# Kernel optimization log

Measured on AMD Instinct MI355X. Metric: run time of the kernel, lower is better.

The kernel has to match this reference:

```python
import jax, jax.numpy as jnp
import numpy as np

B, K, D, H = 4, 2048, 1024, 16
NCTX = K // 2
IMAGE_SIZE = 224
MAX_POS = 1024


def _build_rope_cache_2d(max_pos, dim, base=10000.0):
    half_dim = dim // 2
    theta = 1.0 / base ** (np.arange(0, half_dim, 2, dtype=np.float32) / half_dim)
    positions = np.arange(max_pos, dtype=np.float32)
    freqs = np.outer(positions, theta)  # [max_pos, dim/4]
    return jnp.asarray(np.stack([np.cos(freqs), np.sin(freqs)], axis=-1))  # [max_pos, dim/4, 2]


def apply_rope_2d(x, coords, rope_cache, image_size):
    b, k, d = x.shape
    half, quarter = d // 2, d // 4
    max_pos = rope_cache.shape[0]
    cn = jnp.clip(coords / image_size * (max_pos - 1), 0, max_pos - 1)
    y_pos = cn[..., 0].astype(jnp.int32)
    x_pos = cn[..., 1].astype(jnp.int32)
    y_rope = rope_cache[y_pos]  # [b,k,quarter,2]
    x_rope = rope_cache[x_pos]

    def rot(part, r):
        c, s = r[..., 0], r[..., 1]
        p0, p1 = part[..., 0], part[..., 1]
        return jnp.stack([p0 * c - p1 * s, p0 * s + p1 * c], -1).reshape(b, k, half)

    xp = x[..., :half].reshape(b, k, quarter, 2)
    yp = x[..., half:].reshape(b, k, quarter, 2)
    return jnp.concatenate([rot(xp, x_rope), rot(yp, y_rope)], -1)


def mha(q_tok, kv_tok, in_w, in_b, out_w, out_b, num_heads):
    b, nq, d = q_tok.shape
    hd = d // num_heads
    wq, wk, wv = jnp.split(in_w, 3, axis=0)
    bq, bk, bv = jnp.split(in_b, 3)
    q = (q_tok @ wq.T + bq).reshape(b, nq, num_heads, hd)
    k = (kv_tok @ wk.T + bk).reshape(b, -1, num_heads, hd)
    v = (kv_tok @ wv.T + bv).reshape(b, -1, num_heads, hd)
    s = jnp.einsum('bqhd,bkhd->bhqk', q, k) / jnp.sqrt(jnp.asarray(hd, q.dtype))
    a = jax.nn.softmax(s, axis=-1)
    o = jnp.einsum('bhqk,bkhd->bqhd', a, v).reshape(b, nq, d)
    return o @ out_w.T + out_b


def setup_inputs() -> dict:
    key = jax.random.key(0)
    ks = jax.random.split(key, 12)
    sc = 1.0 / np.sqrt(D)
    x = jax.random.normal(ks[0], (B, K, D), jnp.float32)
    coords = jax.random.uniform(ks[1], (B, K, 2), jnp.float32) * IMAGE_SIZE
    # boolean context mask with exactly NCTX context tokens per batch (code assumes equal counts)
    perms = jax.vmap(lambda k_: jax.random.permutation(k_, K))(jax.random.split(ks[2], B))
    is_context = jax.vmap(lambda m, i: m.at[i].set(True))(jnp.zeros((B, K), bool), perms[:, :NCTX])
    rope_cache = _build_rope_cache_2d(MAX_POS, D)
    return {
        'x': x, 'coords': coords, 'is_context': is_context, 'rope_cache': rope_cache,
        'ctx_in_w': jax.random.normal(ks[3], (3 * D, D), jnp.float32) * sc,
        'ctx_in_b': jnp.zeros((3 * D,), jnp.float32),
        'ctx_out_w': jax.random.normal(ks[4], (D, D), jnp.float32) * sc,
        'ctx_out_b': jnp.zeros((D,), jnp.float32),
        'tgt_in_w': jax.random.normal(ks[5], (3 * D, D), jnp.float32) * sc,
        'tgt_in_b': jnp.zeros((3 * D,), jnp.float32),
        'tgt_out_w': jax.random.normal(ks[6], (D, D), jnp.float32) * sc,
        'tgt_out_b': jnp.zeros((D,), jnp.float32),
    }


def reference(x, coords, is_context, rope_cache,
              ctx_in_w, ctx_in_b, ctx_out_w, ctx_out_b,
              tgt_in_w, tgt_in_b, tgt_out_w, tgt_out_b):
    # 2D RoPE before attention (as in the backbone)
    xr = apply_rope_2d(x, coords, rope_cache, IMAGE_SIZE)
    # stable argsort: context positions (key 0) first, in original order
    order = jnp.argsort(jnp.where(is_context, 0, 1), axis=1, stable=True)
    ctx_idx = order[:, :NCTX]   # [B, NCTX]
    tgt_idx = order[:, NCTX:]   # [B, K-NCTX]
    ctx_tok = jnp.take_along_axis(xr, ctx_idx[..., None], axis=1)
    tgt_tok = jnp.take_along_axis(xr, tgt_idx[..., None], axis=1)
    ctx_out = mha(ctx_tok, ctx_tok, ctx_in_w, ctx_in_b, ctx_out_w, ctx_out_b, H)
    tgt_out = mha(tgt_tok, ctx_tok, tgt_in_w, tgt_in_b, tgt_out_w, tgt_out_b, H)
    out = jnp.zeros_like(x)
    out = jax.vmap(lambda o, i, v: o.at[i].set(v))(out, ctx_idx, ctx_out)
    out = jax.vmap(lambda o, i, v: o.at[i].set(v))(out, tgt_idx, tgt_out)
    return out
```

## Files before the change

### kernel.cpp

```cpp
#include <hip/hip_runtime.h>
#include <math.h>

#define B_    4
#define K_    2048
#define D_    1024
#define H_    16
#define NCTX_ 1024

typedef unsigned short ushort_t;
typedef _Float16 f16;
typedef __attribute__((ext_vector_type(8))) _Float16 f16x8;
typedef __attribute__((ext_vector_type(4))) float f32x4;

union U4 {
  f16 h[4];
  ushort4 u;
};

union P4 {
  f16 h[4];
  ushort4 u;
};

__device__ __forceinline__ void gload16(const void* g, void* l) {
  __builtin_amdgcn_global_load_lds(
      (const __attribute__((address_space(1))) unsigned int*)g,
      (__attribute__((address_space(3))) unsigned int*)l, 16, 0, 0);
}

__global__ __launch_bounds__(256) void partition_kernel(
    const unsigned char* __restrict__ isctx, int* __restrict__ pos,
    int* __restrict__ ipos) {
  const int b = blockIdx.x;
  const int tid = threadIdx.x;
  const int wid = tid >> 6, lane = tid & 63;
  __shared__ int csum[4];
  __shared__ int waveTot[4];
  __shared__ int strideSh;

  int cnt = 0;
  for (int i = 0; i < 32; ++i) cnt += (isctx[tid * 32 + i] != 0);
  for (int off = 32; off; off >>= 1) cnt += __shfl_down(cnt, off, 64);
  if (lane == 0) csum[wid] = cnt;
  __syncthreads();
  if (tid == 0) {
    int t = csum[0] + csum[1] + csum[2] + csum[3];
    strideSh = (t > 2048) ? 1 : ((t > 768) ? 4 : 8);
  }
  __syncthreads();
  const int stride = strideSh;

  const unsigned char* base = isctx + (size_t)b * K_ * stride;
  int f[8];
  int s = 0;
  for (int i = 0; i < 8; ++i) {
    f[i] = base[(size_t)(tid * 8 + i) * stride] != 0;
    s += f[i];
  }
  int inc = s;
  for (int off = 1; off < 64; off <<= 1) {
    int v = __shfl_up(inc, off, 64);
    if (lane >= off) inc += v;
  }
  if (lane == 63) waveTot[wid] = inc;
  __syncthreads();
  int wOff = 0;
  for (int w = 0; w < wid; ++w) wOff += waveTot[w];
  int run = wOff + inc - s;
  for (int i = 0; i < 8; ++i) {
    int k = tid * 8 + i;
    int p;
    if (f[i]) {
      p = run;
      run++;
    } else {
      p = NCTX_ + k - run;
    }
    pos[b * K_ + k] = p;
    ipos[b * K_ + p] = k;
  }
}

__global__ __launch_bounds__(256) void rope_kernel(
    const float* __restrict__ x, const float* __restrict__ coords,
    const float* __restrict__ cache, const int* __restrict__ ipos,
    f16* __restrict__ tok) {
  const int row = blockIdx.x;
  const int b = row >> 11;
  const int r = row & (K_ - 1);
  const int k = ipos[row];
  const int t = threadIdx.x;

  const float cy = coords[(size_t)(b * K_ + k) * 2 + 0];
  const float cx = coords[(size_t)(b * K_ + k) * 2 + 1];
  const int ypos = (int)fminf(fmaxf(cy / 224.0f * 1023.0f, 0.0f), 1023.0f);
  const int xpos = (int)fminf(fmaxf(cx / 224.0f * 1023.0f, 0.0f), 1023.0f);

  const float4 v = ((const float4*)(x + ((size_t)b * K_ + k) * D_))[t];
  const int e = 4 * t;
  const float* crow;
  int coff;
  if (e < 512) {
    crow = cache + (size_t)xpos * 512;
    coff = e;
  } else {
    crow = cache + (size_t)ypos * 512;
    coff = e - 512;
  }
  const float4 cs = *(const float4*)(crow + coff);
  float o[4];
  o[0] = v.x * cs.x - v.y * cs.y;
  o[1] = v.x * cs.y + v.y * cs.x;
  o[2] = v.z * cs.z - v.w * cs.w;
  o[3] = v.z * cs.w + v.w * cs.z;
  U4 h;
#pragma unroll
  for (int i = 0; i < 4; ++i) h.h[i] = (f16)o[i];
  ((ushort4*)(tok + ((size_t)b * K_ + r) * D_))[t] = h.u;
}

__global__ __launch_bounds__(256) void cvt_all(
    const float* __restrict__ ctx_in_w, const float* __restrict__ tgt_in_w,
    const float* __restrict__ ctx_out_w, const float* __restrict__ tgt_out_w,
    f16* __restrict__ dst) {
  const int i4 = blockIdx.x * 256 + threadIdx.x;
  const int f = i4 * 4;
  const float* src;
  if (f < 3145728) src = ctx_in_w + f;
  else if (f < 5242880) src = tgt_in_w + (f - 3145728 + 1048576);
  else if (f < 6291456) src = tgt_in_w + (f - 5242880);
  else if (f < 7340032) src = ctx_out_w + (f - 6291456);
  else src = tgt_out_w + (f - 7340032);
  const float4 v = *(const float4*)src;
  U4 u;
  u.h[0] = (f16)v.x;
  u.h[1] = (f16)v.y;
  u.h[2] = (f16)v.z;
  u.h[3] = (f16)v.w;
  ((ushort4*)dst)[i4] = u.u;
}

#define GEMM_PRE(AP, WP, Kd)                                                  \
  const int rb_ = wave * 8 + (lane >> 3);          \
  const int kk_ = ((lane & 7) ^ (lane >> 3)) * 8;   \
  const f16* gA_ = (AP) + (size_t)rb_ * (Kd) + kk_;                           \
  const f16* gW_ = (WP) + (size_t)rb_ * (Kd) + kk_;                           \
  const int lA_ = wave * 8 * 64 + lane * 8;

#define GEMM_STAGE(k0s, bb)                                                   \
  _Pragma("unroll") for (int j = 0; j < 4; ++j) {                             \
    gload16(gA_ + (size_t)j * 32 * Kd_ + (k0s), &lds[(bb) + j * 2048 + lA_]); \
    gload16(gW_ + (size_t)j * 32 * Kd_ + (k0s),                               \
            &lds[(bb) + 8192 + j * 2048 + lA_]);                              \
  }

#define GEMM_TILE(bb)                                                         \
  _Pragma("unroll") for (int kh = 0; kh < 2; ++kh) {                          \
    f16x8 af[4], wf[4];                                                       \
    _Pragma("unroll") for (int i = 0; i < 4; ++i) {                           \
      const int ca = ((kh * 4 + quad) ^ (m16 & 7)) * 8;                       \
      af[i] = *(const f16x8*)&lds[(bb) + (wm + i * 16 + m16) * 64 + ca];      \
      wf[i] =                                                                 \
          *(const f16x8*)&lds[(bb) + 8192 + (wn + i * 16 + m16) * 64 + ca];   \
    }                                                                         \
    _Pragma("unroll") for (int i = 0; i < 4; ++i)                             \
        _Pragma("unroll") for (int j = 0; j < 4; ++j)                         \
      acc[i][j] = __builtin_amdgcn_mfma_f32_16x16x32_f16(af[i], wf[j],        \
                                                         acc[i][j], 0, 0, 0); \
  }

#define GEMM_CORE(AP, WP, Kd)                                                 \
  f32x4 acc[4][4];                                                            \
  {                                                                           \
    const f32x4 z = {0.f, 0.f, 0.f, 0.f};                                     \
    for (int i = 0; i < 4; ++i)                                               \
      for (int j = 0; j < 4; ++j) acc[i][j] = z;                              \
  }                                                                           \
  const int Kd_ = (Kd);                                                       \
  GEMM_PRE(AP, WP, Kd_)                                                       \
  GEMM_STAGE(0, 0)                                                            \
  for (int t = 0; t < Kd_ / 64; ++t) {                                        \
    const int cb = (t & 1) * 16384;                                           \
    if (t + 1 < Kd_ / 64) {                                                   \
      GEMM_STAGE((t + 1) * 64, ((t + 1) & 1) * 16384)                         \
      asm volatile("s_waitcnt vmcnt(8)" ::: "memory");                        \
    } else {                                                                  \
      asm volatile("s_waitcnt vmcnt(0)" ::: "memory");                        \
    }                                                                         \
    __builtin_amdgcn_s_barrier();                                             \
    asm volatile("" ::: "memory");                                            \
    GEMM_TILE(cb)                                                             \
    asm volatile("" ::: "memory");                                            \
    __builtin_amdgcn_s_barrier();                                             \
  }

__global__ __launch_bounds__(256, 2) void gemm_proj(
    const f16* __restrict__ tok, const f16* __restrict__ wcat,
    const float* __restrict__ ctx_in_b, const float* __restrict__ tgt_in_b,
    f16* __restrict__ qkvc, f16* __restrict__ kvt, f16* __restrict__ qt,
    f16* __restrict__ vtc, f16* __restrict__ vtt) {
  __shared__ f16 lds[32768];
  const int tid = threadIdx.x;
  const int wave = tid >> 6, lane = tid & 63;
  const int quad = lane >> 4, m16 = lane & 15;
  const int nb = blockIdx.x, mb = blockIdx.y, b = blockIdx.z;
  const int wm = (wave & 1) << 6, wn = (wave >> 1) << 6;
  const int m0 = mb * 128;
  const bool isQ = nb >= 40;
  const int n0 = isQ ? (nb - 40) * 128 : nb * 128;
  const f16* AP = tok + (size_t)b * K_ * D_ +
                  (isQ ? (size_t)NCTX_ * D_ : (size_t)0) + (size_t)m0 * D_;
  const f16* WP = wcat + (isQ ? (size_t)5242880 : (size_t)0) +
                  (size_t)n0 * D_;

  GEMM_CORE(AP, WP, D_)

#pragma unroll
  for (int j = 0; j < 4; ++j) {
    const int col = n0 + wn + j * 16 + m16;
    if (isQ) {
      const float bv = tgt_in_b[col];
      f16* dst = qt + (size_t)b * NCTX_ * 1024;
#pragma unroll
      for (int i = 0; i < 4; ++i) {
        const int mr = m0 + wm + i * 16 + quad * 4;
#pragma unroll
        for (int r = 0; r < 4; ++r)
          dst[(size_t)(mr + r) * 1024 + col] = (f16)(acc[i][j][r] + bv);
      }
    } else if (col < 2048) {
      const float bv = ctx_in_b[col];
      f16* dst = qkvc + (size_t)b * NCTX_ * 2048;
#pragma unroll
      for (int i = 0; i < 4; ++i) {
        const int mr = m0 + wm + i * 16 + quad * 4;
#pragma unroll
        for (int r = 0; r < 4; ++r)
          dst[(size_t)(mr + r) * 2048 + col] = (f16)(acc[i][j][r] + bv);
      }
    } else if (col >= 3072 && col < 4096) {
      const float bv = tgt_in_b[D_ + col - 3072];
      f16* dst = kvt + (size_t)b * NCTX_ * 1024;
      const int dcol = col - 3072;
#pragma unroll
      for (int i = 0; i < 4; ++i) {
        const int mr = m0 + wm + i * 16 + quad * 4;
#pragma unroll
        for (int r = 0; r < 4; ++r)
          dst[(size_t)(mr + r) * 1024 + dcol] = (f16)(acc[i][j][r] + bv);
      }
    } else {
      const bool isCtxV = col < 3072;
      const int hd = isCtxV ? (col - 2048) : (col - 4096);
      const float bv = isCtxV ? ctx_in_b[col] : tgt_in_b[D_ + col - 3072];
      f16* dst = (isCtxV ? vtc : vtt) +
                 ((size_t)(b * H_ + (hd >> 6)) << 16) +
                 (size_t)(hd & 63) * 1024;
#pragma unroll
      for (int i = 0; i < 4; ++i) {
        const int mr = m0 + wm + i * 16 + quad * 4;
        P4 p4;
#pragma unroll
        for (int r = 0; r < 4; ++r) p4.h[r] = (f16)(acc[i][j][r] + bv);
        *(ushort4*)(dst + mr) = p4.u;
      }
    }
  }
}

__global__ __launch_bounds__(256, 2) void gemm_out(
    const f16* __restrict__ Atok, const f16* __restrict__ Wbase,
    const float* __restrict__ bias_ctx, const float* __restrict__ bias_tgt,
    const int* __restrict__ ipos, float* __restrict__ out) {
  __shared__ f16 lds[32768];
  const int tid = threadIdx.x;
  const int wave = tid >> 6, lane = tid & 63;
  const int quad = lane >> 4, m16 = lane & 15;
  const int n0 = blockIdx.x * 128, m0 = blockIdx.y * 128;
  const int b = blockIdx.z & 3, sel = blockIdx.z >> 2;
  const int wm = (wave & 1) << 6, wn = (wave >> 1) << 6;
  const f16* AP = Atok + (size_t)b * K_ * D_ + (size_t)sel * NCTX_ * D_ +
                  (size_t)m0 * D_;
  const f16* WP = Wbase + (size_t)sel * 1048576 + (size_t)n0 * D_;
  const float* bias = sel ? bias_tgt : bias_ctx;

  GEMM_CORE(AP, WP, D_)

#pragma unroll
  for (int j = 0; j < 4; ++j) {
    const int col = n0 + wn + j * 16 + m16;
    const float bv = bias[col];
#pragma unroll
    for (int i = 0; i < 4; ++i) {
      const int mr = m0 + wm + i * 16 + quad * 4;
#pragma unroll
      for (int r = 0; r < 4; ++r) {
        const int orow = ipos[b * K_ + sel * NCTX_ + mr + r];
        out[(size_t)b * K_ * D_ + (size_t)orow * D_ + col] =
            acc[i][j][r] + bv;
      }
    }
  }
}

__global__ __launch_bounds__(512) void attn_mfma(
    const f16* __restrict__ qkvc, const f16* __restrict__ kvt,
    const f16* __restrict__ qt, const f16* __restrict__ vtc,
    const f16* __restrict__ vtt, f16* __restrict__ O) {
  __shared__ f16 QP[8192];
  __shared__ f16 Xb[12288];
  const int tid = threadIdx.x, wave = tid >> 6, lane = tid & 63;
  const int quad = lane >> 4, m16 = lane & 15;

  const int id = blockIdx.x;
  const int xcd = id & 7;
  const int t_ = id >> 3;
  const int j_ = t_ & 7;
  const int g = ((t_ >> 3) << 3) + xcd;
  const int h = g & 15;
  const int zz = g >> 4;
  const int b = zz & 3;
  const bool isCtx = zz < 4;
  const int q0 = j_ * 128;

  const f16* Qb;
  const f16* Kb;
  int ld;
  if (isCtx) {
    Qb = qkvc + (size_t)b * NCTX_ * 2048 + h * 64;
    Kb = Qb + 1024;
    ld = 2048;
  } else {
    Qb = qt + (size_t)b * NCTX_ * 1024 + h * 64;
    Kb = kvt + (size_t)b * NCTX_ * 1024 + h * 64;
    ld = 1024;
  }
  const f16* Vb = (isCtx ? vtc : vtt) + ((size_t)(b * H_ + h) << 16);
  f16* Ob = O + (size_t)b * K_ * D_ + (isCtx ? 0 : (size_t)NCTX_ * D_);

  const int rowS = tid >> 3;
  const int kkc = ((tid & 7) ^ (rowS & 7)) * 8;
  const int lB = tid * 8;

#pragma unroll
  for (int j = 0; j < 2; ++j)
    gload16(Qb + (size_t)(q0 + j * 64 + rowS) * ld + kkc, &QP[j * 4096 + lB]);
  gload16(Kb + (size_t)rowS * ld + kkc, &Xb[lB]);
  gload16(Vb + (size_t)rowS * 1024 + kkc, &Xb[4096 + lB]);

  float m_run = -1e30f, l_run = 0.f;
  f32x4 Oa[4];
  const f32x4 z = {0.f, 0.f, 0.f, 0.f};
#pragma unroll
  for (int j = 0; j < 4; ++j) Oa[j] = z;

  asm volatile("s_waitcnt vmcnt(0)" ::: "memory");
  __builtin_amdgcn_s_barrier();

  const int c0 = (quad ^ (m16 & 7)) * 8;
  const int c1 = ((quad + 4) ^ (m16 & 7)) * 8;
  const f16x8 qf0 = *(const f16x8*)&QP[(wave * 16 + m16) * 64 + c0];
  const f16x8 qf1 = *(const f16x8*)&QP[(wave * 16 + m16) * 64 + c1];

  f16* Pw = QP + wave * 1024;

  int xK = 0, xV = 4096;
  for (int kt = 0; kt < 16; ++kt) {
    int xKn = xK + 8192;
    if (xKn >= 12288) xKn -= 12288;

    asm volatile("s_waitcnt vmcnt(0)" ::: "memory");
    __builtin_amdgcn_s_barrier();
    asm volatile("" ::: "memory");
    if (kt < 15)
      gload16(Kb + (size_t)((kt + 1) * 64 + rowS) * ld + kkc, &Xb[xKn + lB]);

    f32x4 S[4];
    __builtin_amdgcn_s_setprio(1);
#pragma unroll
    for (int jn = 0; jn < 4; ++jn) {
      S[jn] = z;
      const f16x8 kf0 = *(const f16x8*)&Xb[xK + (jn * 16 + m16) * 64 + c0];
      const f16x8 kf1 = *(const f16x8*)&Xb[xK + (jn * 16 + m16) * 64 + c1];
      S[jn] = __builtin_amdgcn_mfma_f32_16x16x32_f16(kf0, qf0, S[jn], 0, 0, 0);
      S[jn] = __builtin_amdgcn_mfma_f32_16x16x32_f16(kf1, qf1, S[jn], 0, 0, 0);
    }
    __builtin_amdgcn_s_setprio(0);

    __builtin_amdgcn_s_barrier();
    asm volatile("" ::: "memory");
    if (kt < 15)
      gload16(Vb + (size_t)rowS * 1024 + (kt + 1) * 64 + kkc, &Xb[xK + lB]);

    float mv0 = fmaxf(fmaxf(S[0][0], S[1][0]), fmaxf(S[2][0], S[3][0]));
    float mv1 = fmaxf(fmaxf(S[0][1], S[1][1]), fmaxf(S[2][1], S[3][1]));
    float mv2 = fmaxf(fmaxf(S[0][2], S[1][2]), fmaxf(S[2][2], S[3][2]));
    float mv3 = fmaxf(fmaxf(S[0][3], S[1][3]), fmaxf(S[2][3], S[3][3]));
    float mx = fmaxf(fmaxf(mv0, mv1), fmaxf(mv2, mv3));
    mx = fmaxf(mx, __shfl_xor(mx, 16, 64));
    mx = fmaxf(mx, __shfl_xor(mx, 32, 64));
    mx *= 0.125f;

    const bool grow = !__all(mx <= m_run);
    float al = 1.f;
    if (grow) {
      const float mnew = fmaxf(m_run, mx);
      al = __expf(m_run - mnew);
      m_run = mnew;
    }

    float rs = 0.f;
#pragma unroll
    for (int jn = 0; jn < 4; ++jn) {
      P4 p4;
#pragma unroll
      for (int r = 0; r < 4; ++r) {
        const float p = __expf(__builtin_fmaf(S[jn][r], 0.125f, -m_run));
        rs += p;
        p4.h[r] = (f16)p;
      }
      *(ushort4*)&Pw[m16 * 64 + (((jn * 2 + (quad >> 1)) ^ (m16 & 7)) * 8) +
                     (quad & 1) * 4] = p4.u;
    }
    rs += __shfl_xor(rs, 16, 64);
    rs += __shfl_xor(rs, 32, 64);

    if (grow) {
      l_run = l_run * al + rs;
      float alq[4];
#pragma unroll
      for (int r = 0; r < 4; ++r) alq[r] = __shfl(al, quad * 4 + r, 64);
#pragma unroll
      for (int j = 0; j < 4; ++j) {
        Oa[j][0] *= alq[0];
        Oa[j][1] *= alq[1];
        Oa[j][2] *= alq[2];
        Oa[j][3] *= alq[3];
      }
    } else {
      l_run += rs;
    }

    const f16x8 pf0 = *(const f16x8*)&Pw[m16 * 64 + c0];
    const f16x8 pf1 = *(const f16x8*)&Pw[m16 * 64 + c1];
    __builtin_amdgcn_s_setprio(1);
#pragma unroll
    for (int jd = 0; jd < 4; ++jd) {
      const f16x8 vf0 = *(const f16x8*)&Xb[xV + (jd * 16 + m16) * 64 + c0];
      const f16x8 vf1 = *(const f16x8*)&Xb[xV + (jd * 16 + m16) * 64 + c1];
      Oa[jd] = __builtin_amdgcn_mfma_f32_16x16x32_f16(pf0, vf0, Oa[jd], 0, 0, 0);
      Oa[jd] = __builtin_amdgcn_mfma_f32_16x16x32_f16(pf1, vf1, Oa[jd], 0, 0, 0);
    }
    __builtin_amdgcn_s_setprio(0);

    xV = xK;
    xK = xKn;
  }

  float lq[4];
#pragma unroll
  for (int r = 0; r < 4; ++r) lq[r] = 1.0f / __shfl(l_run, quad * 4 + r, 64);
#pragma unroll
  for (int jd = 0; jd < 4; ++jd)
#pragma unroll
    for (int r = 0; r < 4; ++r) {
      const float v = Oa[jd][r] * lq[r];
      const size_t off = (size_t)(q0 + wave * 16 + quad * 4 + r) * D_ +
                         h * 64 + jd * 16 + m16;
      Ob[off] = (f16)v;
    }
}

extern "C" void kernel_launch(void* const* d_in, const int* in_sizes, int n_in,
                              void* d_out, int out_size, void* d_ws,
                              size_t ws_size, hipStream_t stream) {
  const float* x = (const float*)d_in[0];
  const float* coords = (const float*)d_in[1];
  const unsigned char* isctx = (const unsigned char*)d_in[2];
  const float* rope = (const float*)d_in[3];
  const float* ctx_in_w = (const float*)d_in[4];
  const float* ctx_in_b = (const float*)d_in[5];
  const float* ctx_out_w = (const float*)d_in[6];
  const float* ctx_out_b = (const float*)d_in[7];
  const float* tgt_in_w = (const float*)d_in[8];
  const float* tgt_in_b = (const float*)d_in[9];
  const float* tgt_out_w = (const float*)d_in[10];
  const float* tgt_out_b = (const float*)d_in[11];
  float* out = (float*)d_out;

  f16* ws = (f16*)d_ws;
  f16* tok = ws;
  f16* wcat = tok + 8388608;
  f16* qkvc = wcat + 8388608;
  f16* kvt = qkvc + 8388608;
  f16* qt = kvt + 4194304;
  f16* vtc = qt + 4194304;
  f16* vtt = vtc + 4194304;
  int* pos = (int*)(vtt + 4194304);
  int* ipos = pos + B_ * K_;

  partition_kernel<<<B_, 256, 0, stream>>>(isctx, pos, ipos);
  cvt_all<<<8192, 256, 0, stream>>>(ctx_in_w, tgt_in_w, ctx_out_w, tgt_out_w,
                                    wcat);
  rope_kernel<<<B_ * K_, 256, 0, stream>>>(x, coords, rope, ipos, tok);

  gemm_proj<<<dim3(48, 8, B_), 256, 0, stream>>>(
      tok, wcat, ctx_in_b, tgt_in_b, qkvc, kvt, qt, vtc, vtt);

  attn_mfma<<<dim3(1024, 1, 1), 512, 0, stream>>>(qkvc, kvt, qt, vtc, vtt,
                                                  tok);

  gemm_out<<<dim3(8, 8, 2 * B_), 256, 0, stream>>>(
      tok, wcat + 6291456, ctx_out_b, tgt_out_b, ipos, out);
}
```

Measured before the change: 278.8 us.

## Double-buffer K/V with 128-key tiles in attention kernel

Replaces the rotating three-slot K/V buffer and 64-key steps with separate double buffers for K and V over 128-key tiles. Each iteration prefetches the whole next tile, so only one barrier is needed per iteration instead of two, and the loop runs half as many times. The softmax max and rescale are now computed once per 128 keys. In exchange, LDS use rises from about 40KB to 80KB per block, which may cut occupancy, and more S registers are live at once. The P·V product is still done in two 64-key halves through the same per-wave P scratch.

```diff
diff --git a/kernel.cpp b/kernel.cpp
--- a/kernel.cpp
+++ b/kernel.cpp
@@ -308,7 +308,8 @@
     const f16* __restrict__ qt, const f16* __restrict__ vtc,
     const f16* __restrict__ vtt, f16* __restrict__ O) {
   __shared__ f16 QP[8192];
-  __shared__ f16 Xb[12288];
+  __shared__ f16 KB[2][8192];
+  __shared__ f16 VB[2][8192];
   const int tid = threadIdx.x, wave = tid >> 6, lane = tid & 63;
   const int quad = lane >> 4, m16 = lane & 15;
 
@@ -345,8 +346,11 @@
 #pragma unroll
   for (int j = 0; j < 2; ++j)
     gload16(Qb + (size_t)(q0 + j * 64 + rowS) * ld + kkc, &QP[j * 4096 + lB]);
-  gload16(Kb + (size_t)rowS * ld + kkc, &Xb[lB]);
-  gload16(Vb + (size_t)rowS * 1024 + kkc, &Xb[4096 + lB]);
+#pragma unroll
+  for (int j = 0; j < 2; ++j) {
+    gload16(Kb + (size_t)(j * 64 + rowS) * ld + kkc, &KB[0][j * 4096 + lB]);
+    gload16(Vb + (size_t)rowS * 1024 + j * 64 + kkc, &VB[0][j * 4096 + lB]);
+  }
 
   float m_run = -1e30f, l_run = 0.f;
   f32x4 Oa[4];
@@ -354,7 +358,7 @@
 #pragma unroll
   for (int j = 0; j < 4; ++j) Oa[j] = z;
 
-  asm volatile("s_waitcnt vmcnt(0)" ::: "memory");
+  asm volatile("s_waitcnt vmcnt(4)" ::: "memory");
   __builtin_amdgcn_s_barrier();
 
   const int c0 = (quad ^ (m16 & 7)) * 8;
@@ -364,39 +368,46 @@
 
   f16* Pw = QP + wave * 1024;
 
-  int xK = 0, xV = 4096;
-  for (int kt = 0; kt < 16; ++kt) {
-    int xKn = xK + 8192;
-    if (xKn >= 12288) xKn -= 12288;
+  for (int kt = 0; kt < 8; ++kt) {
+    const int cur = kt & 1;
 
     asm volatile("s_waitcnt vmcnt(0)" ::: "memory");
     __builtin_amdgcn_s_barrier();
     asm volatile("" ::: "memory");
-    if (kt < 15)
-      gload16(Kb + (size_t)((kt + 1) * 64 + rowS) * ld + kkc, &Xb[xKn + lB]);
-
-    f32x4 S[4];
+    if (kt < 7) {
+#pragma unroll
+      for (int j = 0; j < 2; ++j) {
+        gload16(Kb + (size_t)((kt + 1) * 128 + j * 64 + rowS) * ld + kkc,
+                &KB[cur ^ 1][j * 4096 + lB]);
+        gload16(Vb + (size_t)rowS * 1024 + (kt + 1) * 128 + j * 64 + kkc,
+                &VB[cur ^ 1][j * 4096 + lB]);
+      }
+    }
+
+    f32x4 S[8];
     __builtin_amdgcn_s_setprio(1);
 #pragma unroll
-    for (int jn = 0; jn < 4; ++jn) {
+    for (int jn = 0; jn < 8; ++jn) {
       S[jn] = z;
-      const f16x8 kf0 = *(const f16x8*)&Xb[xK + (jn * 16 + m16) * 64 + c0];
-      const f16x8 kf1 = *(const f16x8*)&Xb[xK + (jn * 16 + m16) * 64 + c1];
+      const f16x8 kf0 = *(const f16x8*)&KB[cur][(jn >> 2) * 4096 +
+                                               ((jn & 3) * 16 + m16) * 64 +
+                                               c0];
+      const f16x8 kf1 = *(const f16x8*)&KB[cur][(jn >> 2) * 4096 +
+                                               ((jn & 3) * 16 + m16) * 64 +
+                                               c1];
       S[jn] = __builtin_amdgcn_mfma_f32_16x16x32_f16(kf0, qf0, S[jn], 0, 0, 0);
       S[jn] = __builtin_amdgcn_mfma_f32_16x16x32_f16(kf1, qf1, S[jn], 0, 0, 0);
     }
     __builtin_amdgcn_s_setprio(0);
 
-    __builtin_amdgcn_s_barrier();
-    asm volatile("" ::: "memory");
-    if (kt < 15)
-      gload16(Vb + (size_t)rowS * 1024 + (kt + 1) * 64 + kkc, &Xb[xK + lB]);
-
-    float mv0 = fmaxf(fmaxf(S[0][0], S[1][0]), fmaxf(S[2][0], S[3][0]));
-    float mv1 = fmaxf(fmaxf(S[0][1], S[1][1]), fmaxf(S[2][1], S[3][1]));
-    float mv2 = fmaxf(fmaxf(S[0][2], S[1][2]), fmaxf(S[2][2], S[3][2]));
-    float mv3 = fmaxf(fmaxf(S[0][3], S[1][3]), fmaxf(S[2][3], S[3][3]));
-    float mx = fmaxf(fmaxf(mv0, mv1), fmaxf(mv2, mv3));
+    float mv[4];
+#pragma unroll
+    for (int r = 0; r < 4; ++r) {
+      const float a0 = fmaxf(fmaxf(S[0][r], S[1][r]), fmaxf(S[2][r], S[3][r]));
+      const float a1 = fmaxf(fmaxf(S[4][r], S[5][r]), fmaxf(S[6][r], S[7][r]));
+      mv[r] = fmaxf(a0, a1);
+    }
+    float mx = fmaxf(fmaxf(mv[0], mv[1]), fmaxf(mv[2], mv[3]));
     mx = fmaxf(mx, __shfl_xor(mx, 16, 64));
     mx = fmaxf(mx, __shfl_xor(mx, 32, 64));
     mx *= 0.125f;
@@ -411,17 +422,13 @@
 
     float rs = 0.f;
 #pragma unroll
-    for (int jn = 0; jn < 4; ++jn) {
-      P4 p4;
+    for (int jn = 0; jn < 8; ++jn)
 #pragma unroll
       for (int r = 0; r < 4; ++r) {
         const float p = __expf(__builtin_fmaf(S[jn][r], 0.125f, -m_run));
         rs += p;
-        p4.h[r] = (f16)p;
-      }
-      *(ushort4*)&Pw[m16 * 64 + (((jn * 2 + (quad >> 1)) ^ (m16 & 7)) * 8) +
-                     (quad & 1) * 4] = p4.u;
-    }
+        S[jn][r] = p;
+      }
     rs += __shfl_xor(rs, 16, 64);
     rs += __shfl_xor(rs, 32, 64);
 
@@ -441,20 +448,33 @@
       l_run += rs;
     }
 
-    const f16x8 pf0 = *(const f16x8*)&Pw[m16 * 64 + c0];
-    const f16x8 pf1 = *(const f16x8*)&Pw[m16 * 64 + c1];
-    __builtin_amdgcn_s_setprio(1);
-#pragma unroll
-    for (int jd = 0; jd < 4; ++jd) {
-      const f16x8 vf0 = *(const f16x8*)&Xb[xV + (jd * 16 + m16) * 64 + c0];
-      const f16x8 vf1 = *(const f16x8*)&Xb[xV + (jd * 16 + m16) * 64 + c1];
-      Oa[jd] = __builtin_amdgcn_mfma_f32_16x16x32_f16(pf0, vf0, Oa[jd], 0, 0, 0);
-      Oa[jd] = __builtin_amdgcn_mfma_f32_16x16x32_f16(pf1, vf1, Oa[jd], 0, 0, 0);
-    }
-    __builtin_amdgcn_s_setprio(0);
-
-    xV = xK;
-    xK = xKn;
+#pragma unroll
+    for (int hf = 0; hf < 2; ++hf) {
+#pragma unroll
+      for (int j2 = 0; j2 < 4; ++j2) {
+        const int jn = hf * 4 + j2;
+        P4 p4;
+#pragma unroll
+        for (int r = 0; r < 4; ++r) p4.h[r] = (f16)S[jn][r];
+        *(ushort4*)&Pw[m16 * 64 + (((j2 * 2 + (quad >> 1)) ^ (m16 & 7)) * 8) +
+                       (quad & 1) * 4] = p4.u;
+      }
+      const f16x8 pf0 = *(const f16x8*)&Pw[m16 * 64 + c0];
+      const f16x8 pf1 = *(const f16x8*)&Pw[m16 * 64 + c1];
+      __builtin_amdgcn_s_setprio(1);
+#pragma unroll
+      for (int jd = 0; jd < 4; ++jd) {
+        const f16x8 vf0 = *(const f16x8*)&VB[cur][hf * 4096 +
+                                                 (jd * 16 + m16) * 64 + c0];
+        const f16x8 vf1 = *(const f16x8*)&VB[cur][hf * 4096 +
+                                                 (jd * 16 + m16) * 64 + c1];
+        Oa[jd] =
+            __builtin_amdgcn_mfma_f32_16x16x32_f16(pf0, vf0, Oa[jd], 0, 0, 0);
+        Oa[jd] =
+            __builtin_amdgcn_mfma_f32_16x16x32_f16(pf1, vf1, Oa[jd], 0, 0, 0);
+      }
+      __builtin_amdgcn_s_setprio(0);
+    }
   }
 
   float lq[4];
```

Result: no change. 274.8 us (-1.4%).
